# Kernel optimization log

Measured on AMD Instinct MI355X. Metric: run time of the kernel, lower is better.

Reference implementation:

```python
import jax, jax.numpy as jnp
import numpy as np

D_MODEL = 1024
N_HEADS = 16
HEAD_DIM = D_MODEL // N_HEADS  # 64
LATENT = 256
B, S = 2, 2048


def setup_inputs() -> dict:
    key = jax.random.key(0)
    ks = jax.random.split(key, 13)
    sc = 0.02
    inp = {
        'x': jax.random.normal(ks[0], (B, S, D_MODEL), jnp.float32),
        'Wq': jax.random.normal(ks[1], (D_MODEL, D_MODEL), jnp.float32) * sc,
        'bq': jnp.zeros((D_MODEL,), jnp.float32),
        'Wkd': jax.random.normal(ks[2], (D_MODEL, LATENT), jnp.float32) * sc,
        'bkd': jnp.zeros((LATENT,), jnp.float32),
        'Wvd': jax.random.normal(ks[3], (D_MODEL, LATENT), jnp.float32) * sc,
        'bvd': jnp.zeros((LATENT,), jnp.float32),
        'Wku': jax.random.normal(ks[4], (LATENT, D_MODEL), jnp.float32) * sc,
        'bku': jnp.zeros((D_MODEL,), jnp.float32),
        'Wvu': jax.random.normal(ks[5], (LATENT, D_MODEL), jnp.float32) * sc,
        'bvu': jnp.zeros((D_MODEL,), jnp.float32),
        'Wo': jax.random.normal(ks[6], (D_MODEL, D_MODEL), jnp.float32) * sc,
        'bo': jnp.zeros((D_MODEL,), jnp.float32),
    }
    return inp


def reference(x, Wq, bq, Wkd, bkd, Wvd, bvd, Wku, bku, Wvu, bvu, Wo, bo):
    b, s, _ = x.shape
    # projections
    Q = x @ Wq + bq                      # [b, s, d_model]
    K_latent = x @ Wkd + bkd             # [b, s, latent]
    V_latent = x @ Wvd + bvd             # [b, s, latent]
    K = K_latent @ Wku + bku             # [b, s, d_model]
    V = V_latent @ Wvu + bvu             # [b, s, d_model]
    # split heads
    Qh = Q.reshape(b, s, N_HEADS, HEAD_DIM)
    Kh = K.reshape(b, s, N_HEADS, HEAD_DIM)
    Vh = V.reshape(b, s, N_HEADS, HEAD_DIM)
    scale = 1.0 / jnp.sqrt(jnp.asarray(HEAD_DIM, x.dtype))
    scores = jnp.einsum('bqhd,bkhd->bhqk', Qh, Kh) * scale  # [b,h,s,s]
    attn = jax.nn.softmax(scores, axis=-1)
    ctx = jnp.einsum('bhqk,bkhd->bqhd', attn, Vh).reshape(b, s, D_MODEL)
    out = ctx @ Wo + bo
    return out
```

## Files before the change

kernel.cpp:

```cpp
#include <hip/hip_runtime.h>
#include <hip/hip_bf16.h>
#include <cstddef>

#define B_SZ 2
#define SEQ  2048
#define DM   1024
#define NH   16
#define HD   64
#define LAT  256
#define MTOT (B_SZ*SEQ)
#define NQKV 1536
#define QSCALE 0.18033688011112042f

typedef short bf16x8 __attribute__((ext_vector_type(8)));
typedef float floatx4 __attribute__((ext_vector_type(4)));
typedef float floatx16 __attribute__((ext_vector_type(16)));
typedef unsigned short u16;

#if __has_builtin(__builtin_amdgcn_exp2f)
#define EXP2(x) __builtin_amdgcn_exp2f(x)
#else
#define EXP2(x) exp2f(x)
#endif

__device__ __forceinline__ u16 f2bf(float f) {
  union { float f; unsigned u; } a; a.f = f;
  unsigned r = a.u + 0x7FFFu + ((a.u >> 16) & 1u);
  return (u16)(r >> 16);
}

__device__ __forceinline__ floatx4 mfma16(bf16x8 a, bf16x8 b, floatx4 c) {
  return __builtin_amdgcn_mfma_f32_16x16x32_bf16(a, b, c, 0, 0, 0);
}

__device__ __forceinline__ floatx16 mfma32(bf16x8 a, bf16x8 b, floatx16 c) {
  return __builtin_amdgcn_mfma_f32_32x32x16_bf16(a, b, c, 0, 0, 0);
}

__device__ __forceinline__ void load16(const u16* g, u16* l) {
  __builtin_amdgcn_global_load_lds((const __attribute__((address_space(1))) unsigned*)g,
                                   (__attribute__((address_space(3))) unsigned*)l, 16, 0, 0);
}

__device__ void transpose_tile(const float* __restrict__ W, u16* __restrict__ WT,
                               int K, int N, int k0, int n0, u16 (*t)[65]) {
  const int r = threadIdx.x >> 4;
  const int c4 = (threadIdx.x & 15) * 4;
#pragma unroll
  for (int s = 0; s < 4; s++) {
    int row = s * 16 + r;
    float4 v = *(const float4*)&W[(size_t)(k0 + row) * N + n0 + c4];
    t[row][c4 + 0] = f2bf(v.x); t[row][c4 + 1] = f2bf(v.y);
    t[row][c4 + 2] = f2bf(v.z); t[row][c4 + 3] = f2bf(v.w);
  }
  __syncthreads();
  const int r2 = threadIdx.x >> 2;
  const int c8 = (threadIdx.x & 3) * 16;
  __align__(16) u16 tmp[16];
#pragma unroll
  for (int i = 0; i < 16; i++) tmp[i] = t[c8 + i][r2];
  u16* dst = WT + (size_t)(n0 + r2) * K + k0 + c8;
  *(bf16x8*)dst       = *(const bf16x8*)&tmp[0];
  *(bf16x8*)(dst + 8) = *(const bf16x8*)&tmp[8];
}

__global__ __launch_bounds__(256)
void prep_k(const float* __restrict__ x, u16* __restrict__ xb,
            const float* __restrict__ Wq, const float* __restrict__ Wkd,
            const float* __restrict__ Wvd, const float* __restrict__ Wku,
            const float* __restrict__ Wvu, const float* __restrict__ Wo,
            u16* __restrict__ WstkT, u16* __restrict__ WkuT,
            u16* __restrict__ WvuT, u16* __restrict__ WoT,
            const float* __restrict__ bq, const float* __restrict__ bkd,
            const float* __restrict__ bvd, float* __restrict__ bqkv) {
  __shared__ u16 t[64][65];
  const int blk = blockIdx.x;
  if (blk < 4096) {
    int i = blk * 256 + threadIdx.x;
    float4 v = ((const float4*)x)[i];
    ushort4 o; o.x = f2bf(v.x); o.y = f2bf(v.y); o.z = f2bf(v.z); o.w = f2bf(v.w);
    ((ushort4*)xb)[i] = o;
  } else if (blk < 4352) {
    int tt = blk - 4096;
    transpose_tile(Wq, WstkT, DM, DM, (tt >> 4) * 64, (tt & 15) * 64, t);
  } else if (blk < 4416) {
    int tt = blk - 4352;
    transpose_tile(Wkd, WstkT + (size_t)DM * DM, DM, LAT, (tt >> 2) * 64, (tt & 3) * 64, t);
  } else if (blk < 4480) {
    int tt = blk - 4416;
    transpose_tile(Wvd, WstkT + (size_t)1280 * DM, DM, LAT, (tt >> 2) * 64, (tt & 3) * 64, t);
  } else if (blk < 4544) {
    int tt = blk - 4480;
    transpose_tile(Wku, WkuT, LAT, DM, (tt >> 4) * 64, (tt & 15) * 64, t);
  } else if (blk < 4608) {
    int tt = blk - 4544;
    transpose_tile(Wvu, WvuT, LAT, DM, (tt >> 4) * 64, (tt & 15) * 64, t);
  } else if (blk < 4864) {
    int tt = blk - 4608;
    transpose_tile(Wo, WoT, DM, DM, (tt >> 4) * 64, (tt & 15) * 64, t);
  } else {
    int i = (blk - 4864) * 256 + threadIdx.x;
    float v = (i < 1024) ? bq[i] : (i < 1280) ? bkd[i - 1024] : bvd[i - 1280];
    bqkv[i] = v;
  }
}

template<int TM, int OUT_BF16, int VT1>
__global__ __launch_bounds__(256)
void gemm_bt(const u16* __restrict__ A0, const u16* __restrict__ A1,
             const u16* __restrict__ BT0, const u16* __restrict__ BT1,
             const float* __restrict__ bias0, const float* __restrict__ bias1,
             void* __restrict__ C0, void* __restrict__ C1,
             int M, int N, int Kd, int lda, float qscale, int qcols) {
  constexpr int FM = TM / 32;
  __shared__ u16 As[TM * 64];
  __shared__ u16 Bs[64 * 64];
  const u16* A  = blockIdx.z ? A1 : A0;
  const u16* BT = blockIdx.z ? BT1 : BT0;
  const float* bias = blockIdx.z ? bias1 : bias0;
  void* C = blockIdx.z ? C1 : C0;

  const int tid = threadIdx.x;
  const int m0 = blockIdx.y * TM, n0 = blockIdx.x * 64;
  const int wave = tid >> 6, lane = tid & 63;
  const int l15 = lane & 15, quad = lane >> 4;
  const int wm = (wave >> 1) * (TM / 2), wn = (wave & 1) * 32;

  floatx4 acc[FM][2];
#pragma unroll
  for (int i = 0; i < FM; i++)
#pragma unroll
    for (int j = 0; j < 2; j++) acc[i][j] = (floatx4){0.f, 0.f, 0.f, 0.f};

  const int tr = tid >> 3;
  const int tc8 = (tid & 7) * 8;
  const u16* Ag = A  + (size_t)(m0 + tr) * lda + tc8;
  const u16* Bg = BT + (size_t)(n0 + tr) * Kd + tc8;
  u16* AsW = &As[(size_t)tid * 8];
  u16* BsW = &Bs[(size_t)tid * 8];

  for (int k0 = 0; k0 < Kd; k0 += 64) {
    __syncthreads();
#pragma unroll
    for (int s = 0; s < FM; s++)
      load16(Ag + (size_t)(s * 32) * lda + k0, AsW + s * 2048);
#pragma unroll
    for (int s = 0; s < 2; s++)
      load16(Bg + (size_t)(s * 32) * Kd  + k0, BsW + s * 2048);
    __syncthreads();
#pragma unroll
    for (int kk = 0; kk < 2; kk++) {
      bf16x8 af[FM], bfr[2];
#pragma unroll
      for (int i = 0; i < FM; i++)
        af[i]  = *(const bf16x8*)&As[(wm + i * 16 + l15) * 64 + kk * 32 + quad * 8];
#pragma unroll
      for (int j = 0; j < 2; j++)
        bfr[j] = *(const bf16x8*)&Bs[(wn + j * 16 + l15) * 64 + kk * 32 + quad * 8];
#pragma unroll
      for (int i = 0; i < FM; i++)
#pragma unroll
        for (int j = 0; j < 2; j++)
          acc[i][j] = mfma16(af[i], bfr[j], acc[i][j]);
    }
  }

  if (VT1 && blockIdx.z == 1) {
#pragma unroll
    for (int i = 0; i < FM; i++) {
      int row = m0 + wm + i * 16 + quad * 4;
      int bb = row >> 11, sb = row & 2047;
#pragma unroll
      for (int j = 0; j < 2; j++) {
        int col = n0 + wn + j * 16 + l15;
        float bv = bias[col];
        union { u16 u[4]; uint2 w2; } tv;
#pragma unroll
        for (int r = 0; r < 4; r++) tv.u[r] = f2bf(acc[i][j][r] + bv);
        *(uint2*)((u16*)C + ((size_t)(bb * 16 + (col >> 6)) * 64 + (col & 63)) * SEQ + sb) = tv.w2;
      }
    }
  } else {
#pragma unroll
    for (int i = 0; i < FM; i++) {
      int row = m0 + wm + i * 16 + quad * 4;
#pragma unroll
      for (int j = 0; j < 2; j++) {
        int col = n0 + wn + j * 16 + l15;
        float bv = bias[col];
        float sc = (col < qcols) ? qscale : 1.f;
#pragma unroll
        for (int r = 0; r < 4; r++) {
          float v = (acc[i][j][r] + bv) * sc;
          if (OUT_BF16) ((u16*)C)[(size_t)(row + r) * N + col] = f2bf(v);
          else          ((float*)C)[(size_t)(row + r) * N + col] = v;
        }
      }
    }
  }
}

__global__ __launch_bounds__(256, 2)
void attn_fused(const u16* __restrict__ Q, const u16* __restrict__ K,
                const u16* __restrict__ VT, u16* __restrict__ CTX) {
  __shared__ float Ocmb[64][68];
  __shared__ float Lw[4][64];
  const int lin = blockIdx.y * gridDim.x + blockIdx.x;
  const int idx = lin >> 3;
  const int bh = (lin & 7) * 4 + (idx >> 5);
  const int q0 = (idx & 31) * 64;
  const int b = bh >> 4, h = bh & 15;
  const int wave = threadIdx.x >> 6, lane = threadIdx.x & 63;
  const int l31 = lane & 31;
  const int hi = lane >> 5;

  bf16x8 qf[2][4];
  {
    const u16* Qp = Q + (size_t)(b * SEQ + q0 + l31) * NQKV + h * HD + hi * 8;
#pragma unroll
    for (int qh = 0; qh < 2; qh++)
#pragma unroll
      for (int dc = 0; dc < 4; dc++)
        qf[qh][dc] = *(const bf16x8*)(Qp + (size_t)(qh * 32) * NQKV + dc * 16);
  }
  const u16* Kp = K + ((size_t)(b * SEQ) + l31) * DM + h * HD + hi * 8;
  const u16* Vp = VT + ((size_t)bh * HD + l31) * SEQ + hi * 8;

  floatx16 o[2][2];
  const floatx16 zf16 = {0.f,0.f,0.f,0.f,0.f,0.f,0.f,0.f,0.f,0.f,0.f,0.f,0.f,0.f,0.f,0.f};
#pragma unroll
  for (int dh = 0; dh < 2; dh++)
#pragma unroll
    for (int qh = 0; qh < 2; qh++) o[dh][qh] = zf16;
  float ls[2] = {0.f, 0.f};

  const int kb0 = wave * 512;

  bf16x8 kfb[2][4], vfb[2][2][2];
#pragma unroll
  for (int dc = 0; dc < 4; dc++)
    kfb[0][dc] = *(const bf16x8*)(Kp + (size_t)kb0 * DM + dc * 16);
#pragma unroll
  for (int dh = 0; dh < 2; dh++)
#pragma unroll
    for (int kh = 0; kh < 2; kh++)
      vfb[0][dh][kh] = *(const bf16x8*)(Vp + (size_t)(dh * 32) * SEQ + kb0 + kh * 16);

#pragma unroll 2
  for (int it = 0; it < 16; ++it) {
    const int cur = it & 1, nxt = cur ^ 1;
    const int kb = kb0 + it * 32;
    if (it < 15) {
      const int kn = kb + 32;
#pragma unroll
      for (int dc = 0; dc < 4; dc++)
        kfb[nxt][dc] = *(const bf16x8*)(Kp + (size_t)kn * DM + dc * 16);
#pragma unroll
      for (int dh = 0; dh < 2; dh++)
#pragma unroll
        for (int kh = 0; kh < 2; kh++)
          vfb[nxt][dh][kh] = *(const bf16x8*)(Vp + (size_t)(dh * 32) * SEQ + kn + kh * 16);
    }
#pragma unroll
    for (int qh = 0; qh < 2; qh++) {
      floatx16 z = zf16;
      __builtin_amdgcn_s_setprio(1);
#pragma unroll
      for (int dc = 0; dc < 4; dc++)
        z = mfma32(kfb[cur][dc], qf[qh][dc], z);
      __builtin_amdgcn_s_setprio(0);
      float p[16];
#pragma unroll
      for (int r = 0; r < 16; r++) p[r] = EXP2(z[r]);
      ls[qh] += (((p[0] + p[1]) + (p[2] + p[3])) + ((p[4] + p[5]) + (p[6] + p[7])))
              + (((p[8] + p[9]) + (p[10] + p[11])) + ((p[12] + p[13]) + (p[14] + p[15])));
      unsigned wt[8];
#pragma unroll
      for (int i = 0; i < 8; i++) {
        unsigned ua = __float_as_uint(p[2 * i]) + 0x8000u;
        unsigned ub = __float_as_uint(p[2 * i + 1]) + 0x8000u;
        wt[i] = __builtin_amdgcn_perm(ub, ua, 0x07060302u);
      }
      unsigned sx[8];
#pragma unroll
      for (int i = 0; i < 8; i++) sx[i] = (unsigned)__shfl_xor((int)wt[i], 32);
      union { unsigned u[4]; bf16x8 v; } b0, b1;
      b0.u[0] = hi ? sx[2] : wt[0];
      b0.u[1] = hi ? sx[3] : wt[1];
      b0.u[2] = hi ? wt[2] : sx[0];
      b0.u[3] = hi ? wt[3] : sx[1];
      b1.u[0] = hi ? sx[6] : wt[4];
      b1.u[1] = hi ? sx[7] : wt[5];
      b1.u[2] = hi ? wt[6] : sx[4];
      b1.u[3] = hi ? wt[7] : sx[5];
      __builtin_amdgcn_s_setprio(1);
#pragma unroll
      for (int dh = 0; dh < 2; dh++) {
        o[dh][qh] = mfma32(vfb[cur][dh][0], b0.v, o[dh][qh]);
        o[dh][qh] = mfma32(vfb[cur][dh][1], b1.v, o[dh][qh]);
      }
      __builtin_amdgcn_s_setprio(0);
    }
  }

#pragma unroll
  for (int qh = 0; qh < 2; qh++) {
    float v = ls[qh];
    v += __shfl_xor(v, 32);
    if (hi == 0) Lw[wave][qh * 32 + l31] = v;
  }
  if (wave == 0) {
#pragma unroll
    for (int dh = 0; dh < 2; dh++)
#pragma unroll
      for (int qh = 0; qh < 2; qh++)
#pragma unroll
        for (int g = 0; g < 4; g++) {
          floatx4 t = {o[dh][qh][4 * g], o[dh][qh][4 * g + 1],
                       o[dh][qh][4 * g + 2], o[dh][qh][4 * g + 3]};
          *(floatx4*)&Ocmb[qh * 32 + l31][dh * 32 + g * 8 + hi * 4] = t;
        }
  }
  __syncthreads();
  if (wave == 1) {
#pragma unroll
    for (int dh = 0; dh < 2; dh++)
#pragma unroll
      for (int qh = 0; qh < 2; qh++)
#pragma unroll
        for (int g = 0; g < 4; g++) {
          floatx4* pp = (floatx4*)&Ocmb[qh * 32 + l31][dh * 32 + g * 8 + hi * 4];
          floatx4 t = {o[dh][qh][4 * g], o[dh][qh][4 * g + 1],
                       o[dh][qh][4 * g + 2], o[dh][qh][4 * g + 3]};
          *pp = *pp + t;
        }
  }
  __syncthreads();
  if (wave == 2) {
#pragma unroll
    for (int dh = 0; dh < 2; dh++)
#pragma unroll
      for (int qh = 0; qh < 2; qh++)
#pragma unroll
        for (int g = 0; g < 4; g++) {
          floatx4* pp = (floatx4*)&Ocmb[qh * 32 + l31][dh * 32 + g * 8 + hi * 4];
          floatx4 t = {o[dh][qh][4 * g], o[dh][qh][4 * g + 1],
                       o[dh][qh][4 * g + 2], o[dh][qh][4 * g + 3]};
          *pp = *pp + t;
        }
  }
  __syncthreads();
  if (wave == 3) {
#pragma unroll
    for (int qh = 0; qh < 2; qh++) {
      int qq = qh * 32 + l31;
      float lt = Lw[0][qq] + Lw[1][qq] + Lw[2][qq] + Lw[3][qq];
      float inv = 1.f / lt;
      u16* Crow = CTX + (size_t)(b * SEQ + q0 + qq) * DM + h * HD + hi * 4;
#pragma unroll
      for (int dh = 0; dh < 2; dh++)
#pragma unroll
        for (int g = 0; g < 4; g++) {
          const float* oc = &Ocmb[qq][dh * 32 + g * 8 + hi * 4];
          union { u16 u[4]; uint2 w2; } tv;
#pragma unroll
          for (int r = 0; r < 4; r++)
            tv.u[r] = f2bf((o[dh][qh][4 * g + r] + oc[r]) * inv);
          *(uint2*)(Crow + dh * 32 + g * 8) = tv.w2;
        }
    }
  }
}

extern "C" void kernel_launch(void* const* d_in, const int* in_sizes, int n_in,
                              void* d_out, int out_size, void* d_ws, size_t ws_size,
                              hipStream_t stream) {
  const float* x   = (const float*)d_in[0];
  const float* Wq  = (const float*)d_in[1];
  const float* bq  = (const float*)d_in[2];
  const float* Wkd = (const float*)d_in[3];
  const float* bkd = (const float*)d_in[4];
  const float* Wvd = (const float*)d_in[5];
  const float* bvd = (const float*)d_in[6];
  const float* Wku = (const float*)d_in[7];
  const float* bku = (const float*)d_in[8];
  const float* Wvu = (const float*)d_in[9];
  const float* bvu = (const float*)d_in[10];
  const float* Wo  = (const float*)d_in[11];
  const float* bo  = (const float*)d_in[12];
  float* out = (float*)d_out;

  float* bqkv = (float*)d_ws;
  u16* p = (u16*)((char*)d_ws + 1536 * sizeof(float));
  u16* xb    = p; p += (size_t)MTOT * DM;
  u16* WstkT = p; p += (size_t)NQKV * DM;
  u16* WkuT  = p; p += (size_t)DM * LAT;
  u16* WvuT  = p; p += (size_t)DM * LAT;
  u16* WoT   = p; p += (size_t)DM * DM;
  u16* QKVb  = p; p += (size_t)MTOT * NQKV;
  u16* Kb    = p; p += (size_t)MTOT * DM;
  u16* VTb   = p; p += (size_t)MTOT * DM;
  u16* CXb   = p; p += (size_t)MTOT * DM;

  prep_k<<<4870, 256, 0, stream>>>(x, xb, Wq, Wkd, Wvd, Wku, Wvu, Wo,
                                   WstkT, WkuT, WvuT, WoT, bq, bkd, bvd, bqkv);

  gemm_bt<128, 1, 0><<<dim3(NQKV / 64, MTOT / 128, 1), 256, 0, stream>>>(
      xb, xb, WstkT, WstkT, bqkv, bqkv, QKVb, QKVb, MTOT, NQKV, DM, DM, QSCALE, DM);
  gemm_bt<128, 1, 1><<<dim3(DM / 64, MTOT / 128, 2), 256, 0, stream>>>(
      QKVb + 1024, QKVb + 1280, WkuT, WvuT, bku, bvu, Kb, VTb, MTOT, DM, LAT, NQKV, 1.f, 0);

  attn_fused<<<dim3(SEQ / 64, B_SZ * NH), 256, 0, stream>>>(QKVb, Kb, VTb, CXb);

  gemm_bt<64, 0, 0><<<dim3(DM / 64, MTOT / 64, 1), 256, 0, stream>>>(
      CXb, CXb, WoT, WoT, bo, bo, out, out, MTOT, DM, DM, DM, 1.f, 0);
}
```

Baseline: 224.7 us.

## Stage K/V tiles in shared memory across 8 waves with 128-query blocks

Restructures the attention kernel into 512-thread blocks covering 128 queries. Four query-waves each share K/V tiles staged cooperatively into double-buffered, XOR-swizzled LDS, and two key-split halves are merged at the end. Previously each wave loaded its own K/V fragments straight from global memory for a 64-query tile. This raises K/V reuse across queries and cuts global traffic, at the cost of a __syncthreads per 64-key step and LDS read overhead. It also halves register accumulators per wave, which allows higher occupancy (launch bounds 512,4).

```diff
diff --git a/kernel.cpp b/kernel.cpp
--- a/kernel.cpp
+++ b/kernel.cpp
@@ -200,80 +200,83 @@
   }
 }
 
-__global__ __launch_bounds__(256, 2)
+__global__ __launch_bounds__(512, 4)
 void attn_fused(const u16* __restrict__ Q, const u16* __restrict__ K,
                 const u16* __restrict__ VT, u16* __restrict__ CTX) {
-  __shared__ float Ocmb[64][68];
-  __shared__ float Lw[4][64];
+  __shared__ __align__(16) u16 KVt[2][2][2][64][64];
   const int lin = blockIdx.y * gridDim.x + blockIdx.x;
   const int idx = lin >> 3;
-  const int bh = (lin & 7) * 4 + (idx >> 5);
-  const int q0 = (idx & 31) * 64;
+  const int bh = (lin & 7) * 4 + (idx >> 4);
+  const int q0 = (idx & 15) * 128;
   const int b = bh >> 4, h = bh & 15;
   const int wave = threadIdx.x >> 6, lane = threadIdx.x & 63;
+  const int qw = wave & 3;
+  const int kw = wave >> 2;
   const int l31 = lane & 31;
   const int hi = lane >> 5;
-
-  bf16x8 qf[2][4];
+  const int lr = lane >> 3;
+  const int cx = (lane & 7) ^ lr;
+
+  bf16x8 qf[4];
   {
-    const u16* Qp = Q + (size_t)(b * SEQ + q0 + l31) * NQKV + h * HD + hi * 8;
-#pragma unroll
-    for (int qh = 0; qh < 2; qh++)
+    const u16* Qp = Q + (size_t)(b * SEQ + q0 + qw * 32 + l31) * NQKV + h * HD + hi * 8;
+#pragma unroll
+    for (int dc = 0; dc < 4; dc++)
+      qf[dc] = *(const bf16x8*)(Qp + dc * 16);
+  }
+
+  const u16* Ksrc[2];
+  const u16* Vsrc[2];
+#pragma unroll
+  for (int s = 0; s < 2; s++) {
+    int r = qw * 16 + s * 8 + lr;
+    Ksrc[s] = K + (size_t)(b * SEQ + r) * DM + h * HD + cx * 8;
+    Vsrc[s] = VT + ((size_t)bh * HD + r) * SEQ + cx * 8;
+  }
+
+  floatx16 o[2];
+  const floatx16 zf16 = {0.f,0.f,0.f,0.f,0.f,0.f,0.f,0.f,0.f,0.f,0.f,0.f,0.f,0.f,0.f,0.f};
+  o[0] = zf16; o[1] = zf16;
+  float ls = 0.f;
+
+  {
+    const int ktb = kw * 1024;
+#pragma unroll
+    for (int s = 0; s < 2; s++) {
+      load16(Ksrc[s] + (size_t)ktb * DM, &KVt[0][kw][0][qw * 16 + s * 8][0]);
+      load16(Vsrc[s] + ktb,              &KVt[1][kw][0][qw * 16 + s * 8][0]);
+    }
+  }
+  __syncthreads();
+
+#pragma unroll 2
+  for (int t = 0; t < 16; ++t) {
+    const int cur = t & 1, nxt = cur ^ 1;
+    if (t < 15) {
+      const int ktb = kw * 1024 + (t + 1) * 64;
+#pragma unroll
+      for (int s = 0; s < 2; s++) {
+        load16(Ksrc[s] + (size_t)ktb * DM, &KVt[0][kw][nxt][qw * 16 + s * 8][0]);
+        load16(Vsrc[s] + ktb,              &KVt[1][kw][nxt][qw * 16 + s * 8][0]);
+      }
+    }
+#pragma unroll
+    for (int kh = 0; kh < 2; kh++) {
+      const int rk = kh * 32 + l31;
+      bf16x8 kf[4];
 #pragma unroll
       for (int dc = 0; dc < 4; dc++)
-        qf[qh][dc] = *(const bf16x8*)(Qp + (size_t)(qh * 32) * NQKV + dc * 16);
-  }
-  const u16* Kp = K + ((size_t)(b * SEQ) + l31) * DM + h * HD + hi * 8;
-  const u16* Vp = VT + ((size_t)bh * HD + l31) * SEQ + hi * 8;
-
-  floatx16 o[2][2];
-  const floatx16 zf16 = {0.f,0.f,0.f,0.f,0.f,0.f,0.f,0.f,0.f,0.f,0.f,0.f,0.f,0.f,0.f,0.f};
-#pragma unroll
-  for (int dh = 0; dh < 2; dh++)
-#pragma unroll
-    for (int qh = 0; qh < 2; qh++) o[dh][qh] = zf16;
-  float ls[2] = {0.f, 0.f};
-
-  const int kb0 = wave * 512;
-
-  bf16x8 kfb[2][4], vfb[2][2][2];
-#pragma unroll
-  for (int dc = 0; dc < 4; dc++)
-    kfb[0][dc] = *(const bf16x8*)(Kp + (size_t)kb0 * DM + dc * 16);
-#pragma unroll
-  for (int dh = 0; dh < 2; dh++)
-#pragma unroll
-    for (int kh = 0; kh < 2; kh++)
-      vfb[0][dh][kh] = *(const bf16x8*)(Vp + (size_t)(dh * 32) * SEQ + kb0 + kh * 16);
-
-#pragma unroll 2
-  for (int it = 0; it < 16; ++it) {
-    const int cur = it & 1, nxt = cur ^ 1;
-    const int kb = kb0 + it * 32;
-    if (it < 15) {
-      const int kn = kb + 32;
-#pragma unroll
-      for (int dc = 0; dc < 4; dc++)
-        kfb[nxt][dc] = *(const bf16x8*)(Kp + (size_t)kn * DM + dc * 16);
-#pragma unroll
-      for (int dh = 0; dh < 2; dh++)
-#pragma unroll
-        for (int kh = 0; kh < 2; kh++)
-          vfb[nxt][dh][kh] = *(const bf16x8*)(Vp + (size_t)(dh * 32) * SEQ + kn + kh * 16);
-    }
-#pragma unroll
-    for (int qh = 0; qh < 2; qh++) {
+        kf[dc] = *(const bf16x8*)&KVt[0][kw][cur][rk][((dc * 2 + hi) ^ (l31 & 7)) * 8];
       floatx16 z = zf16;
       __builtin_amdgcn_s_setprio(1);
 #pragma unroll
-      for (int dc = 0; dc < 4; dc++)
-        z = mfma32(kfb[cur][dc], qf[qh][dc], z);
+      for (int dc = 0; dc < 4; dc++) z = mfma32(kf[dc], qf[dc], z);
       __builtin_amdgcn_s_setprio(0);
       float p[16];
 #pragma unroll
       for (int r = 0; r < 16; r++) p[r] = EXP2(z[r]);
-      ls[qh] += (((p[0] + p[1]) + (p[2] + p[3])) + ((p[4] + p[5]) + (p[6] + p[7])))
-              + (((p[8] + p[9]) + (p[10] + p[11])) + ((p[12] + p[13]) + (p[14] + p[15])));
+      ls += (((p[0] + p[1]) + (p[2] + p[3])) + ((p[4] + p[5]) + (p[6] + p[7])))
+          + (((p[8] + p[9]) + (p[10] + p[11])) + ((p[12] + p[13]) + (p[14] + p[15])));
       unsigned wt[8];
 #pragma unroll
       for (int i = 0; i < 8; i++) {
@@ -293,82 +296,53 @@
       b1.u[1] = hi ? sx[7] : wt[5];
       b1.u[2] = hi ? wt[6] : sx[4];
       b1.u[3] = hi ? wt[7] : sx[5];
+      bf16x8 vf[4];
+#pragma unroll
+      for (int j = 0; j < 4; j++) {
+        const int dh = j >> 1, ksl = j & 1;
+        const int rv = dh * 32 + l31;
+        vf[j] = *(const bf16x8*)&KVt[1][kw][cur][rv][((kh * 4 + ksl * 2 + hi) ^ (l31 & 7)) * 8];
+      }
       __builtin_amdgcn_s_setprio(1);
 #pragma unroll
       for (int dh = 0; dh < 2; dh++) {
-        o[dh][qh] = mfma32(vfb[cur][dh][0], b0.v, o[dh][qh]);
-        o[dh][qh] = mfma32(vfb[cur][dh][1], b1.v, o[dh][qh]);
+        o[dh] = mfma32(vf[dh * 2 + 0], b0.v, o[dh]);
+        o[dh] = mfma32(vf[dh * 2 + 1], b1.v, o[dh]);
       }
       __builtin_amdgcn_s_setprio(0);
     }
-  }
-
-#pragma unroll
-  for (int qh = 0; qh < 2; qh++) {
-    float v = ls[qh];
-    v += __shfl_xor(v, 32);
-    if (hi == 0) Lw[wave][qh * 32 + l31] = v;
-  }
-  if (wave == 0) {
+    __syncthreads();
+  }
+
+  float* Osh = (float*)&KVt[0][0][0][0][0];
+  float* Lsh = Osh + 128 * 68;
+  const float lsum = ls + __shfl_xor(ls, 32);
+  const int q = qw * 32 + l31;
+  if (kw == 1) {
 #pragma unroll
     for (int dh = 0; dh < 2; dh++)
 #pragma unroll
-      for (int qh = 0; qh < 2; qh++)
-#pragma unroll
-        for (int g = 0; g < 4; g++) {
-          floatx4 t = {o[dh][qh][4 * g], o[dh][qh][4 * g + 1],
-                       o[dh][qh][4 * g + 2], o[dh][qh][4 * g + 3]};
-          *(floatx4*)&Ocmb[qh * 32 + l31][dh * 32 + g * 8 + hi * 4] = t;
-        }
+      for (int g = 0; g < 4; g++) {
+        floatx4 tv = {o[dh][4 * g], o[dh][4 * g + 1], o[dh][4 * g + 2], o[dh][4 * g + 3]};
+        *(floatx4*)&Osh[q * 68 + dh * 32 + g * 8 + hi * 4] = tv;
+      }
+    if (hi == 0) Lsh[q] = lsum;
   }
   __syncthreads();
-  if (wave == 1) {
+  if (kw == 0) {
+    float inv = 1.f / (lsum + Lsh[q]);
+    u16* Crow = CTX + (size_t)(b * SEQ + q0 + q) * DM + h * HD + hi * 4;
 #pragma unroll
     for (int dh = 0; dh < 2; dh++)
 #pragma unroll
-      for (int qh = 0; qh < 2; qh++)
-#pragma unroll
-        for (int g = 0; g < 4; g++) {
-          floatx4* pp = (floatx4*)&Ocmb[qh * 32 + l31][dh * 32 + g * 8 + hi * 4];
-          floatx4 t = {o[dh][qh][4 * g], o[dh][qh][4 * g + 1],
-                       o[dh][qh][4 * g + 2], o[dh][qh][4 * g + 3]};
-          *pp = *pp + t;
-        }
-  }
-  __syncthreads();
-  if (wave == 2) {
-#pragma unroll
-    for (int dh = 0; dh < 2; dh++)
-#pragma unroll
-      for (int qh = 0; qh < 2; qh++)
-#pragma unroll
-        for (int g = 0; g < 4; g++) {
-          floatx4* pp = (floatx4*)&Ocmb[qh * 32 + l31][dh * 32 + g * 8 + hi * 4];
-          floatx4 t = {o[dh][qh][4 * g], o[dh][qh][4 * g + 1],
-                       o[dh][qh][4 * g + 2], o[dh][qh][4 * g + 3]};
-          *pp = *pp + t;
-        }
-  }
-  __syncthreads();
-  if (wave == 3) {
-#pragma unroll
-    for (int qh = 0; qh < 2; qh++) {
-      int qq = qh * 32 + l31;
-      float lt = Lw[0][qq] + Lw[1][qq] + Lw[2][qq] + Lw[3][qq];
-      float inv = 1.f / lt;
-      u16* Crow = CTX + (size_t)(b * SEQ + q0 + qq) * DM + h * HD + hi * 4;
-#pragma unroll
-      for (int dh = 0; dh < 2; dh++)
-#pragma unroll
-        for (int g = 0; g < 4; g++) {
-          const float* oc = &Ocmb[qq][dh * 32 + g * 8 + hi * 4];
-          union { u16 u[4]; uint2 w2; } tv;
-#pragma unroll
-          for (int r = 0; r < 4; r++)
-            tv.u[r] = f2bf((o[dh][qh][4 * g + r] + oc[r]) * inv);
-          *(uint2*)(Crow + dh * 32 + g * 8) = tv.w2;
-        }
-    }
+      for (int g = 0; g < 4; g++) {
+        const float* oc = &Osh[q * 68 + dh * 32 + g * 8 + hi * 4];
+        union { u16 u[4]; uint2 w2; } tv;
+#pragma unroll
+        for (int r = 0; r < 4; r++)
+          tv.u[r] = f2bf((o[dh][4 * g + r] + oc[r]) * inv);
+        *(uint2*)(Crow + dh * 32 + g * 8) = tv.w2;
+      }
   }
 }
 
@@ -410,7 +384,7 @@
   gemm_bt<128, 1, 1><<<dim3(DM / 64, MTOT / 128, 2), 256, 0, stream>>>(
       QKVb + 1024, QKVb + 1280, WkuT, WvuT, bku, bvu, Kb, VTb, MTOT, DM, LAT, NQKV, 1.f, 0);
 
-  attn_fused<<<dim3(SEQ / 64, B_SZ * NH), 256, 0, stream>>>(QKVb, Kb, VTb, CXb);
+  attn_fused<<<dim3(SEQ / 128, B_SZ * NH), 512, 0, stream>>>(QKVb, Kb, VTb, CXb);
 
   gemm_bt<64, 0, 0><<<dim3(DM / 64, MTOT / 64, 1), 256, 0, stream>>>(
       CXb, CXb, WoT, WoT, bo, bo, out, out, MTOT, DM, DM, DM, 1.f, 0);
```

After: 331.8 us. 1.48x slower.
